# Optimization experiments

Hardware: AMD Instinct MI355X
Metric: run time of the kernel (lower is better)

Reference implementation:

```python
import jax, jax.numpy as jnp
import numpy as np

N_NODES = 50000
N_EDGES = 800000
F_IN = 64
HID = 128
N_GRAPHS = 64
F_OUT = 1
NEG_SLOPE = 0.2


def _glorot(key, shape):
    fan_in, fan_out = shape[0], shape[-1]
    s = jnp.sqrt(6.0 / (fan_in + fan_out))
    return jax.random.uniform(key, shape, jnp.float32, -s, s)


def setup_inputs() -> dict:
    key = jax.random.key(0)
    ks = jax.random.split(key, 24)
    inp = {
        "x": jax.random.normal(ks[0], (N_NODES, F_IN), jnp.float32),
        "edge_index": jax.random.randint(ks[1], (2, N_EDGES), 0, N_NODES, jnp.int32),
        "edge_weight": jax.random.uniform(ks[2], (N_EDGES, 1), jnp.float32),
        "batch": jnp.sort(jax.random.randint(ks[3], (N_NODES,), 0, N_GRAPHS, jnp.int32)),
        # GATv2Conv layer 1 (heads=1): lin_l, lin_r (with bias), lin_edge (no bias), att, out-bias
        "W1l": _glorot(ks[4], (F_IN, HID)), "b1l": jnp.zeros((HID,), jnp.float32),
        "W1r": _glorot(ks[5], (F_IN, HID)), "b1r": jnp.zeros((HID,), jnp.float32),
        "We1": _glorot(ks[6], (1, HID)),
        "att1": _glorot(ks[7], (HID, 1))[:, 0],
        "bias1": jnp.zeros((HID,), jnp.float32),
        # GATv2Conv layer 2
        "W2l": _glorot(ks[8], (HID, HID)), "b2l": jnp.zeros((HID,), jnp.float32),
        "W2r": _glorot(ks[9], (HID, HID)), "b2r": jnp.zeros((HID,), jnp.float32),
        "We2": _glorot(ks[10], (1, HID)),
        "att2": _glorot(ks[11], (HID, 1))[:, 0],
        "bias2": jnp.zeros((HID,), jnp.float32),
        # final Linear
        "Wlin": _glorot(ks[12], (HID, F_OUT)),
        "blin": jnp.zeros((F_OUT,), jnp.float32),
    }
    return inp


def gatv2_layer(x, src, dst, eattr, Wl, bl, Wr, br, We, att, bias):
    n = x.shape[0]
    # add_self_loops=True with edge_attr fill_value='mean'
    loop = jnp.arange(n, dtype=src.dtype)
    src = jnp.concatenate([src, loop])
    dst = jnp.concatenate([dst, loop])
    mean_attr = jnp.mean(eattr, axis=0, keepdims=True)  # [1, edge_dim]
    eattr = jnp.concatenate([eattr, jnp.broadcast_to(mean_attr, (n, eattr.shape[1]))])
    xl = x @ Wl + bl            # [N, HID] source transform
    xr = x @ Wr + br            # [N, HID] dest transform
    ee = eattr @ We             # [E', HID] edge embedding
    m = jax.nn.leaky_relu(xl[src] + xr[dst] + ee, NEG_SLOPE)  # [E', HID]
    logits = m @ att            # [E']
    # per-destination softmax (every node has a self loop, so no empty segments)
    lmax = jax.ops.segment_max(logits, dst, num_segments=n)
    w = jnp.exp(logits - lmax[dst])
    denom = jax.ops.segment_sum(w, dst, num_segments=n)
    alpha = w / denom[dst]
    out = jax.ops.segment_sum(xl[src] * alpha[:, None], dst, num_segments=n)
    return out + bias


def reference(x, edge_index, edge_weight, batch,
              W1l, b1l, W1r, b1r, We1, att1, bias1,
              W2l, b2l, W2r, b2r, We2, att2, bias2,
              Wlin, blin):
    src, dst = edge_index[0], edge_index[1]
    h = jax.nn.relu(gatv2_layer(x, src, dst, edge_weight, W1l, b1l, W1r, b1r, We1, att1, bias1))
    h = jax.nn.relu(gatv2_layer(h, src, dst, edge_weight, W2l, b2l, W2r, b2r, We2, att2, bias2))
    # global_mean_pool over graph assignment
    sums = jax.ops.segment_sum(h, batch, num_segments=N_GRAPHS)
    cnt = jax.ops.segment_sum(jnp.ones((h.shape[0],), h.dtype), batch, num_segments=N_GRAPHS)
    pooled = sums / jnp.maximum(cnt, 1.0)[:, None]
    return pooled @ Wlin + blin  # [N_GRAPHS, F_OUT]
```

## Files before the change

### kernel.cpp

```cpp
#include <hip/hip_runtime.h>

#define NN 50000
#define NE 800000
#define EP (NE + NN)
#define HID 128
#define FIN 64
#define NG 64
#define SLOPE 0.2f
#define NB 49

typedef unsigned short ushort_t;
typedef unsigned int uint_t;

__device__ __forceinline__ float wred_sum(float v) {
  for (int off = 32; off; off >>= 1) v += __shfl_xor(v, off);
  return v;
}
__device__ __forceinline__ ushort_t f2bf(float f) {
  uint_t b = __float_as_uint(f);
  b += 0x7fffu + ((b >> 16) & 1u);
  return (ushort_t)(b >> 16);
}

#define FMA4(A_, S_, W_) \
  A_.x += (S_) * W_.x; A_.y += (S_) * W_.y; \
  A_.z += (S_) * W_.z; A_.w += (S_) * W_.w;

__global__ void k_hist2(const int* __restrict__ edst, const float* __restrict__ ew,
                        int* __restrict__ counts, float* __restrict__ meansum) {
  int tid = blockIdx.x * blockDim.x + threadIdx.x;
  int stride = gridDim.x * blockDim.x;
  float s = 0.f;
  for (int i = tid; i < NE; i += stride) {
    atomicAdd(&counts[edst[i]], 1);
    s += ew[i];
  }
  s = wred_sum(s);
  if ((threadIdx.x & 63) == 0) atomicAdd(meansum, s);
}

__global__ __launch_bounds__(1024) void k_scan1(const int* __restrict__ counts,
                                                int* __restrict__ starts,
                                                int* __restrict__ bsum) {
  __shared__ int wsum[16];
  __shared__ int woff[16];
  int t = threadIdx.x, lane = t & 63, w = t >> 6;
  int i = blockIdx.x * 1024 + t;
  int v = (i < NN) ? counts[i] + 1 : 0;
  int sc = v;
  #pragma unroll
  for (int d = 1; d < 64; d <<= 1) {
    int u = __shfl_up(sc, d);
    if (lane >= d) sc += u;
  }
  if (lane == 63) wsum[w] = sc;
  __syncthreads();
  if (w == 0 && lane < 16) {
    int x = wsum[lane];
    #pragma unroll
    for (int d = 1; d < 16; d <<= 1) {
      int u = __shfl_up(x, d);
      if (lane >= d) x += u;
    }
    woff[lane] = x;
  }
  __syncthreads();
  int waveoff = (w == 0) ? 0 : woff[w - 1];
  if (i < NN) starts[i] = waveoff + sc - v;
  if (t == 1023) bsum[blockIdx.x] = woff[15];
}

__global__ void k_scan2(int* __restrict__ bsum, int* __restrict__ starts) {
  int t = threadIdx.x;
  int v = (t < NB) ? bsum[t] : 0;
  int sc = v;
  #pragma unroll
  for (int d = 1; d < 64; d <<= 1) {
    int u = __shfl_up(sc, d);
    if (t >= d) sc += u;
  }
  if (t < NB) bsum[t] = sc - v;
  if (t == 0) starts[NN] = EP;
}

__global__ __launch_bounds__(1024) void k_scan3(int* __restrict__ starts,
                                                const int* __restrict__ bsum,
                                                int* __restrict__ counts) {
  int i = blockIdx.x * 1024 + threadIdx.x;
  if (i < NN) {
    starts[i] += bsum[blockIdx.x];
    counts[i] = 0;
  }
}

__global__ void k_scatter(const int* __restrict__ esrc, const int* __restrict__ edst,
                          const float* __restrict__ ew, const float* __restrict__ meansum,
                          const int* __restrict__ starts, int* __restrict__ cursor,
                          int2* __restrict__ emeta) {
  float mw = meansum[0] * (1.0f / NE);
  int tid = blockIdx.x * blockDim.x + threadIdx.x;
  int stride = gridDim.x * blockDim.x;
  for (int i = tid; i < EP; i += stride) {
    int s, d; float wv;
    if (i < NE) { s = esrc[i]; d = edst[i]; wv = ew[i]; }
    else        { s = d = i - NE; wv = mw; }
    int pos = starts[d] + atomicAdd(&cursor[d], 1);
    emeta[pos] = make_int2(s, __float_as_int(wv));
  }
}

template <int K>
__global__ __launch_bounds__(256) void k_gemm2(const float* __restrict__ A,
                                               const float* __restrict__ Wl,
                                               const float* __restrict__ bl,
                                               const float* __restrict__ Wr,
                                               const float* __restrict__ br,
                                               ushort_t* __restrict__ xlout,
                                               float* __restrict__ xrout, int n) {
  __shared__ float As[64][K];
  int t = threadIdx.x;
  int nb = blockIdx.x * 64;
  constexpr int F4 = 16 * K;
  for (int i = t; i < F4; i += 256) {
    int row = i / (K / 4);
    int c = (i % (K / 4)) * 4;
    int gn = nb + row;
    float4 v = make_float4(0.f, 0.f, 0.f, 0.f);
    if (gn < n) v = *(const float4*)(A + (size_t)gn * K + c);
    *(float4*)&As[row][c] = v;
  }
  __syncthreads();
  int fx = (t & 31) * 4;
  int ny = (t >> 5) * 8;
  float4 accL[8], accR[8];
  #pragma unroll
  for (int j = 0; j < 8; ++j) {
    accL[j] = make_float4(0.f, 0.f, 0.f, 0.f);
    accR[j] = make_float4(0.f, 0.f, 0.f, 0.f);
  }
  for (int k4 = 0; k4 < K; k4 += 4) {
    float4 wl0 = *(const float4*)(Wl + (size_t)(k4 + 0) * HID + fx);
    float4 wl1 = *(const float4*)(Wl + (size_t)(k4 + 1) * HID + fx);
    float4 wl2 = *(const float4*)(Wl + (size_t)(k4 + 2) * HID + fx);
    float4 wl3 = *(const float4*)(Wl + (size_t)(k4 + 3) * HID + fx);
    float4 wr0 = *(const float4*)(Wr + (size_t)(k4 + 0) * HID + fx);
    float4 wr1 = *(const float4*)(Wr + (size_t)(k4 + 1) * HID + fx);
    float4 wr2 = *(const float4*)(Wr + (size_t)(k4 + 2) * HID + fx);
    float4 wr3 = *(const float4*)(Wr + (size_t)(k4 + 3) * HID + fx);
    #pragma unroll
    for (int j = 0; j < 8; ++j) {
      float4 a = *(const float4*)&As[ny + j][k4];
      FMA4(accL[j], a.x, wl0); FMA4(accL[j], a.y, wl1);
      FMA4(accL[j], a.z, wl2); FMA4(accL[j], a.w, wl3);
      FMA4(accR[j], a.x, wr0); FMA4(accR[j], a.y, wr1);
      FMA4(accR[j], a.z, wr2); FMA4(accR[j], a.w, wr3);
    }
  }
  float4 bbl = *(const float4*)(bl + fx);
  float4 bbr = *(const float4*)(br + fx);
  #pragma unroll
  for (int j = 0; j < 8; ++j) {
    int gn = nb + ny + j;
    if (gn < n) {
      ushort4 u4;
      u4.x = f2bf(accL[j].x + bbl.x); u4.y = f2bf(accL[j].y + bbl.y);
      u4.z = f2bf(accL[j].z + bbl.z); u4.w = f2bf(accL[j].w + bbl.w);
      *(ushort4*)(xlout + (size_t)gn * HID + fx) = u4;
      float4 o = make_float4(accR[j].x + bbr.x, accR[j].y + bbr.y,
                             accR[j].z + bbr.z, accR[j].w + bbr.w);
      *(float4*)(xrout + (size_t)gn * HID + fx) = o;
    }
  }
}

__global__ __launch_bounds__(256, 4) void k_fused(const ushort_t* __restrict__ xl16,
                                                  const float* __restrict__ xr,
                                                  const int2* __restrict__ emeta,
                                                  const int* __restrict__ starts,
                                                  const float* __restrict__ We,
                                                  const float* __restrict__ att,
                                                  const float* __restrict__ bias,
                                                  float* __restrict__ hout) {
  int node = blockIdx.x * (blockDim.x >> 6) + (threadIdx.x >> 6);
  int lane = threadIdx.x & 63;
  if (node >= NN) return;
  int hl = lane & 31;
  int half = lane >> 5;
  int s0 = starts[node], s1 = starts[node + 1];
  int f = hl * 4;
  float4 xro = *(const float4*)(xr + (size_t)node * HID + f);
  float4 we  = *(const float4*)(We + f);
  float4 at  = *(const float4*)(att + f);

  int emy = 8 * half + ((hl >> 2) & 7);
  bool b4 = (hl & 16) != 0;
  bool b3 = (hl & 8) != 0;
  bool b2 = (hl & 4) != 0;

  float ssum = 0.f;
  float4 acc = make_float4(0.f, 0.f, 0.f, 0.f);

  for (int i0 = s0; i0 < s1; i0 += 16) {
    int base = i0 + 8 * half;
    uint2 g[8];
    float p[8];
    #pragma unroll
    for (int k = 0; k < 8; ++k) {
      int idx = min(base + k, s1 - 1);
      int2 em = emeta[idx];
      p[k] = __int_as_float(em.y);
      g[k] = *(const uint2*)(xl16 + (size_t)em.x * HID + f);
    }
    #pragma unroll
    for (int k = 0; k < 8; ++k) {
      float wk = p[k];
      float t0 = __uint_as_float(g[k].x << 16)          + xro.x + wk * we.x;
      float t1 = __uint_as_float(g[k].x & 0xffff0000u)  + xro.y + wk * we.y;
      float t2 = __uint_as_float(g[k].y << 16)          + xro.z + wk * we.z;
      float t3 = __uint_as_float(g[k].y & 0xffff0000u)  + xro.w + wk * we.w;
      t0 = t0 > 0.f ? t0 : SLOPE * t0;
      t1 = t1 > 0.f ? t1 : SLOPE * t1;
      t2 = t2 > 0.f ? t2 : SLOPE * t2;
      t3 = t3 > 0.f ? t3 : SLOPE * t3;
      p[k] = t0 * at.x + t1 * at.y + t2 * at.z + t3 * at.w;
    }
    float sdv, rcv;
    float q0, q1, q2, q3;
    sdv = b4 ? p[0] : p[4]; rcv = __shfl_xor(sdv, 16, 32); q0 = (b4 ? p[4] : p[0]) + rcv;
    sdv = b4 ? p[1] : p[5]; rcv = __shfl_xor(sdv, 16, 32); q1 = (b4 ? p[5] : p[1]) + rcv;
    sdv = b4 ? p[2] : p[6]; rcv = __shfl_xor(sdv, 16, 32); q2 = (b4 ? p[6] : p[2]) + rcv;
    sdv = b4 ? p[3] : p[7]; rcv = __shfl_xor(sdv, 16, 32); q3 = (b4 ? p[7] : p[3]) + rcv;
    float r0, r1;
    sdv = b3 ? q0 : q2; rcv = __shfl_xor(sdv, 8, 32); r0 = (b3 ? q2 : q0) + rcv;
    sdv = b3 ? q1 : q3; rcv = __shfl_xor(sdv, 8, 32); r1 = (b3 ? q3 : q1) + rcv;
    sdv = b2 ? r0 : r1; rcv = __shfl_xor(sdv, 4, 32);
    float lg = (b2 ? r1 : r0) + rcv;
    lg += __shfl_xor(lg, 1, 32);
    lg += __shfl_xor(lg, 2, 32);
    float w = (i0 + emy < s1) ? __expf(lg) : 0.f;
    ssum += w;
    #pragma unroll
    for (int k = 0; k < 8; ++k) {
      float wk = __shfl(w, k << 2, 32);
      acc.x += wk * __uint_as_float(g[k].x << 16);
      acc.y += wk * __uint_as_float(g[k].x & 0xffff0000u);
      acc.z += wk * __uint_as_float(g[k].y << 16);
      acc.w += wk * __uint_as_float(g[k].y & 0xffff0000u);
    }
  }
  acc.x += __shfl_xor(acc.x, 32);
  acc.y += __shfl_xor(acc.y, 32);
  acc.z += __shfl_xor(acc.z, 32);
  acc.w += __shfl_xor(acc.w, 32);
  float st = wred_sum(ssum) * 0.25f;
  float inv = 1.0f / st;
  if (half == 0) {
    float4 bb = *(const float4*)(bias + f);
    float4 o;
    o.x = fmaxf(acc.x * inv + bb.x, 0.f);
    o.y = fmaxf(acc.y * inv + bb.y, 0.f);
    o.z = fmaxf(acc.z * inv + bb.z, 0.f);
    o.w = fmaxf(acc.w * inv + bb.w, 0.f);
    *(float4*)(hout + (size_t)node * HID + f) = o;
  }
}

__global__ void k_bounds(const int* __restrict__ batch, int* __restrict__ gs) {
  int i = blockIdx.x * blockDim.x + threadIdx.x;
  if (i >= NN) return;
  int b = batch[i];
  if (i == 0) {
    for (int g = 0; g <= b; ++g) gs[g] = 0;
  }
  int bn = (i + 1 < NN) ? batch[i + 1] : NG;
  for (int g = b + 1; g <= bn; ++g) gs[g] = i + 1;
}

__global__ __launch_bounds__(256) void k_pool(const float* __restrict__ h,
                                              const int* __restrict__ gs,
                                              const float* __restrict__ Wlin,
                                              const float* __restrict__ blin,
                                              float* __restrict__ out) {
  __shared__ float red[256];
  int g = blockIdx.x;
  int t = threadIdx.x;
  int f = t & 127;
  int half = t >> 7;
  int n0 = gs[g], n1 = gs[g + 1];
  float s0 = 0.f, s1 = 0.f, s2 = 0.f, s3 = 0.f;
  int n = n0 + half;
  for (; n + 6 < n1; n += 8) {
    s0 += h[(size_t)n * HID + f];
    s1 += h[(size_t)(n + 2) * HID + f];
    s2 += h[(size_t)(n + 4) * HID + f];
    s3 += h[(size_t)(n + 6) * HID + f];
  }
  for (; n < n1; n += 2) s0 += h[(size_t)n * HID + f];
  red[t] = (s0 + s1) + (s2 + s3);
  __syncthreads();
  if (t < 128) {
    float pooled = red[t] + red[t + 128];
    float cnt = (float)max(n1 - n0, 1);
    red[t] = (pooled / cnt) * Wlin[f];
  }
  __syncthreads();
  if (t < 64) {
    float v = red[t] + red[t + 64];
    v = wred_sum(v);
    if (t == 0) out[g] = v + blin[0];
  }
}

extern "C" void kernel_launch(void* const* d_in, const int* in_sizes, int n_in,
                              void* d_out, int out_size, void* d_ws, size_t ws_size,
                              hipStream_t stream) {
  const float* x     = (const float*)d_in[0];
  const int*   ei    = (const int*)d_in[1];
  const float* ew    = (const float*)d_in[2];
  const int*   batch = (const int*)d_in[3];
  const float* W1l = (const float*)d_in[4];
  const float* b1l = (const float*)d_in[5];
  const float* W1r = (const float*)d_in[6];
  const float* b1r = (const float*)d_in[7];
  const float* We1 = (const float*)d_in[8];
  const float* at1 = (const float*)d_in[9];
  const float* bi1 = (const float*)d_in[10];
  const float* W2l = (const float*)d_in[11];
  const float* b2l = (const float*)d_in[12];
  const float* W2r = (const float*)d_in[13];
  const float* b2r = (const float*)d_in[14];
  const float* We2 = (const float*)d_in[15];
  const float* at2 = (const float*)d_in[16];
  const float* bi2 = (const float*)d_in[17];
  const float* Wlin = (const float*)d_in[18];
  const float* blin = (const float*)d_in[19];

  float* ws = (float*)d_ws;
  size_t o = 0;
  float*    xr    = ws + o; o += (size_t)NN * HID;
  float*    hb    = ws + o; o += (size_t)NN * HID;
  ushort_t* xl16  = (ushort_t*)(ws + o); o += (size_t)NN * HID / 2;
  int2*     emeta = (int2*)(ws + o); o += (size_t)2 * EP;
  int*      starts = (int*)(ws + o); o += NN + 1;
  int*      gs     = (int*)(ws + o); o += NG + 1;
  int*      bsum   = (int*)(ws + o); o += NB;
  size_t zoff = o;
  int*      counts  = (int*)(ws + o); o += NN;
  float*    meansum = ws + o; o += 1;
  size_t zero_bytes = (o - zoff) * sizeof(float);

  hipMemsetAsync(counts, 0, zero_bytes, stream);

  k_hist2<<<1024, 256, 0, stream>>>(ei + NE, ew, counts, meansum);
  k_scan1<<<NB, 1024, 0, stream>>>(counts, starts, bsum);
  k_scan2<<<1, 64, 0, stream>>>(bsum, starts);
  k_scan3<<<NB, 1024, 0, stream>>>(starts, bsum, counts);
  k_scatter<<<1024, 256, 0, stream>>>(ei, ei + NE, ew, meansum, starts, counts,
                                      emeta);
  k_bounds<<<(NN + 255) / 256, 256, 0, stream>>>(batch, gs);

  int gb  = (NN + 63) / 64;
  int nbn = (NN + 3) / 4;

  k_gemm2<FIN><<<gb, 256, 0, stream>>>(x, W1l, b1l, W1r, b1r, xl16, xr, NN);
  k_fused<<<nbn, 256, 0, stream>>>(xl16, xr, emeta, starts, We1, at1, bi1, hb);
  k_gemm2<HID><<<gb, 256, 0, stream>>>(hb, W2l, b2l, W2r, b2r, xl16, xr, NN);
  k_fused<<<nbn, 256, 0, stream>>>(xl16, xr, emeta, starts, We2, at2, bi2, hb);
  k_pool<<<NG, 256, 0, stream>>>(hb, gs, Wlin, blin, (float*)d_out);
}
```

Before: 405.6 us.

## Use bf16 MFMA for node transforms and store hidden activations in bf16

Replaces the fp32 SIMT GEMM computing xl/xr with a bf16 MFMA 16x16x32 kernel. Inputs are converted to bf16 and the weights are packed into a K-blocked layout by small preprocessing kernels. Layer outputs h are now stored as bf16, which halves the traffic for the second GEMM and for pooling. The cost is lower precision and extra conversion and pack launches, and the epilogue now writes scalar, non-vectorized stores.

```diff
diff --git a/kernel.cpp b/kernel.cpp
--- a/kernel.cpp
+++ b/kernel.cpp
@@ -11,6 +11,8 @@
 
 typedef unsigned short ushort_t;
 typedef unsigned int uint_t;
+typedef __attribute__((ext_vector_type(8))) short bf16x8;
+typedef __attribute__((ext_vector_type(4))) float f32x4;
 
 __device__ __forceinline__ float wred_sum(float v) {
   for (int off = 32; off; off >>= 1) v += __shfl_xor(v, off);
@@ -21,10 +23,25 @@
   b += 0x7fffu + ((b >> 16) & 1u);
   return (ushort_t)(b >> 16);
 }
-
-#define FMA4(A_, S_, W_) \
-  A_.x += (S_) * W_.x; A_.y += (S_) * W_.y; \
-  A_.z += (S_) * W_.z; A_.w += (S_) * W_.w;
+__device__ __forceinline__ float bf2f(ushort_t u) {
+  return __uint_as_float((uint_t)u << 16);
+}
+
+__global__ void k_cvt(const float* __restrict__ x, ushort_t* __restrict__ x16) {
+  int i = blockIdx.x * blockDim.x + threadIdx.x;
+  float4 v = *(const float4*)(x + (size_t)i * 4);
+  ushort4 u;
+  u.x = f2bf(v.x); u.y = f2bf(v.y); u.z = f2bf(v.z); u.w = f2bf(v.w);
+  *(ushort4*)(x16 + (size_t)i * 4) = u;
+}
+
+__global__ void k_packW(const float* __restrict__ W, ushort_t* __restrict__ WP,
+                        int K) {
+  int i = blockIdx.x * blockDim.x + threadIdx.x;
+  if (i >= K * HID) return;
+  int k = i / HID, nn = i % HID;
+  WP[((size_t)(k >> 5) * HID + nn) * 32 + (k & 31)] = f2bf(W[i]);
+}
 
 __global__ void k_hist2(const int* __restrict__ edst, const float* __restrict__ ew,
                         int* __restrict__ counts, float* __restrict__ meansum) {
@@ -110,65 +127,46 @@
 }
 
 template <int K>
-__global__ __launch_bounds__(256) void k_gemm2(const float* __restrict__ A,
-                                               const float* __restrict__ Wl,
+__global__ __launch_bounds__(256) void k_gemmM(const ushort_t* __restrict__ A16,
+                                               const ushort_t* __restrict__ WPl,
                                                const float* __restrict__ bl,
-                                               const float* __restrict__ Wr,
+                                               const ushort_t* __restrict__ WPr,
                                                const float* __restrict__ br,
                                                ushort_t* __restrict__ xlout,
                                                float* __restrict__ xrout, int n) {
-  __shared__ float As[64][K];
   int t = threadIdx.x;
-  int nb = blockIdx.x * 64;
-  constexpr int F4 = 16 * K;
-  for (int i = t; i < F4; i += 256) {
-    int row = i / (K / 4);
-    int c = (i % (K / 4)) * 4;
-    int gn = nb + row;
-    float4 v = make_float4(0.f, 0.f, 0.f, 0.f);
-    if (gn < n) v = *(const float4*)(A + (size_t)gn * K + c);
-    *(float4*)&As[row][c] = v;
-  }
-  __syncthreads();
-  int fx = (t & 31) * 4;
-  int ny = (t >> 5) * 8;
-  float4 accL[8], accR[8];
-  #pragma unroll
-  for (int j = 0; j < 8; ++j) {
-    accL[j] = make_float4(0.f, 0.f, 0.f, 0.f);
-    accR[j] = make_float4(0.f, 0.f, 0.f, 0.f);
-  }
-  for (int k4 = 0; k4 < K; k4 += 4) {
-    float4 wl0 = *(const float4*)(Wl + (size_t)(k4 + 0) * HID + fx);
-    float4 wl1 = *(const float4*)(Wl + (size_t)(k4 + 1) * HID + fx);
-    float4 wl2 = *(const float4*)(Wl + (size_t)(k4 + 2) * HID + fx);
-    float4 wl3 = *(const float4*)(Wl + (size_t)(k4 + 3) * HID + fx);
-    float4 wr0 = *(const float4*)(Wr + (size_t)(k4 + 0) * HID + fx);
-    float4 wr1 = *(const float4*)(Wr + (size_t)(k4 + 1) * HID + fx);
-    float4 wr2 = *(const float4*)(Wr + (size_t)(k4 + 2) * HID + fx);
-    float4 wr3 = *(const float4*)(Wr + (size_t)(k4 + 3) * HID + fx);
-    #pragma unroll
-    for (int j = 0; j < 8; ++j) {
-      float4 a = *(const float4*)&As[ny + j][k4];
-      FMA4(accL[j], a.x, wl0); FMA4(accL[j], a.y, wl1);
-      FMA4(accL[j], a.z, wl2); FMA4(accL[j], a.w, wl3);
-      FMA4(accR[j], a.x, wr0); FMA4(accR[j], a.y, wr1);
-      FMA4(accR[j], a.z, wr2); FMA4(accR[j], a.w, wr3);
-    }
-  }
-  float4 bbl = *(const float4*)(bl + fx);
-  float4 bbr = *(const float4*)(br + fx);
-  #pragma unroll
-  for (int j = 0; j < 8; ++j) {
-    int gn = nb + ny + j;
-    if (gn < n) {
-      ushort4 u4;
-      u4.x = f2bf(accL[j].x + bbl.x); u4.y = f2bf(accL[j].y + bbl.y);
-      u4.z = f2bf(accL[j].z + bbl.z); u4.w = f2bf(accL[j].w + bbl.w);
-      *(ushort4*)(xlout + (size_t)gn * HID + fx) = u4;
-      float4 o = make_float4(accR[j].x + bbr.x, accR[j].y + bbr.y,
-                             accR[j].z + bbr.z, accR[j].w + bbr.w);
-      *(float4*)(xrout + (size_t)gn * HID + fx) = o;
+  int wave = t >> 6, lane = t & 63;
+  int m = lane & 15, kb = lane >> 4;
+  int row0 = blockIdx.x * 64 + wave * 16;
+  int ra = min(row0 + m, n - 1);
+  f32x4 acc[16];
+  #pragma unroll
+  for (int i = 0; i < 16; ++i) acc[i] = (f32x4)(0.f);
+  #pragma unroll
+  for (int kt = 0; kt < K / 32; ++kt) {
+    bf16x8 a = *(const bf16x8*)(A16 + (size_t)ra * K + kt * 32 + kb * 8);
+    #pragma unroll
+    for (int nf = 0; nf < 8; ++nf) {
+      bf16x8 bfr = *(const bf16x8*)(WPl + ((size_t)kt * HID + nf * 16 + m) * 32 + kb * 8);
+      acc[nf] = __builtin_amdgcn_mfma_f32_16x16x32_bf16(a, bfr, acc[nf], 0, 0, 0);
+    }
+    #pragma unroll
+    for (int nf = 0; nf < 8; ++nf) {
+      bf16x8 bfr = *(const bf16x8*)(WPr + ((size_t)kt * HID + nf * 16 + m) * 32 + kb * 8);
+      acc[8 + nf] = __builtin_amdgcn_mfma_f32_16x16x32_bf16(a, bfr, acc[8 + nf], 0, 0, 0);
+    }
+  }
+  #pragma unroll
+  for (int nf = 0; nf < 8; ++nf) {
+    int col = nf * 16 + m;
+    float bbl = bl[col], bbr = br[col];
+    #pragma unroll
+    for (int j = 0; j < 4; ++j) {
+      int r = row0 + kb * 4 + j;
+      if (r < n) {
+        xlout[(size_t)r * HID + col] = f2bf(acc[nf][j] + bbl);
+        xrout[(size_t)r * HID + col] = acc[8 + nf][j] + bbr;
+      }
     }
   }
 }
@@ -180,7 +178,7 @@
                                                   const float* __restrict__ We,
                                                   const float* __restrict__ att,
                                                   const float* __restrict__ bias,
-                                                  float* __restrict__ hout) {
+                                                  ushort_t* __restrict__ hout) {
   int node = blockIdx.x * (blockDim.x >> 6) + (threadIdx.x >> 6);
   int lane = threadIdx.x & 63;
   if (node >= NN) return;
@@ -256,12 +254,12 @@
   float inv = 1.0f / st;
   if (half == 0) {
     float4 bb = *(const float4*)(bias + f);
-    float4 o;
-    o.x = fmaxf(acc.x * inv + bb.x, 0.f);
-    o.y = fmaxf(acc.y * inv + bb.y, 0.f);
-    o.z = fmaxf(acc.z * inv + bb.z, 0.f);
-    o.w = fmaxf(acc.w * inv + bb.w, 0.f);
-    *(float4*)(hout + (size_t)node * HID + f) = o;
+    ushort4 u;
+    u.x = f2bf(fmaxf(acc.x * inv + bb.x, 0.f));
+    u.y = f2bf(fmaxf(acc.y * inv + bb.y, 0.f));
+    u.z = f2bf(fmaxf(acc.z * inv + bb.z, 0.f));
+    u.w = f2bf(fmaxf(acc.w * inv + bb.w, 0.f));
+    *(ushort4*)(hout + (size_t)node * HID + f) = u;
   }
 }
 
@@ -276,7 +274,7 @@
   for (int g = b + 1; g <= bn; ++g) gs[g] = i + 1;
 }
 
-__global__ __launch_bounds__(256) void k_pool(const float* __restrict__ h,
+__global__ __launch_bounds__(256) void k_pool(const ushort_t* __restrict__ h,
                                               const int* __restrict__ gs,
                                               const float* __restrict__ Wlin,
                                               const float* __restrict__ blin,
@@ -290,12 +288,12 @@
   float s0 = 0.f, s1 = 0.f, s2 = 0.f, s3 = 0.f;
   int n = n0 + half;
   for (; n + 6 < n1; n += 8) {
-    s0 += h[(size_t)n * HID + f];
-    s1 += h[(size_t)(n + 2) * HID + f];
-    s2 += h[(size_t)(n + 4) * HID + f];
-    s3 += h[(size_t)(n + 6) * HID + f];
-  }
-  for (; n < n1; n += 2) s0 += h[(size_t)n * HID + f];
+    s0 += bf2f(h[(size_t)n * HID + f]);
+    s1 += bf2f(h[(size_t)(n + 2) * HID + f]);
+    s2 += bf2f(h[(size_t)(n + 4) * HID + f]);
+    s3 += bf2f(h[(size_t)(n + 6) * HID + f]);
+  }
+  for (; n < n1; n += 2) s0 += bf2f(h[(size_t)n * HID + f]);
   red[t] = (s0 + s1) + (s2 + s3);
   __syncthreads();
   if (t < 128) {
@@ -338,8 +336,13 @@
   float* ws = (float*)d_ws;
   size_t o = 0;
   float*    xr    = ws + o; o += (size_t)NN * HID;
-  float*    hb    = ws + o; o += (size_t)NN * HID;
   ushort_t* xl16  = (ushort_t*)(ws + o); o += (size_t)NN * HID / 2;
+  ushort_t* hb16  = (ushort_t*)(ws + o); o += (size_t)NN * HID / 2;
+  ushort_t* x16   = (ushort_t*)(ws + o); o += (size_t)NN * FIN / 2;
+  ushort_t* WP1l  = (ushort_t*)(ws + o); o += (size_t)FIN * HID / 2;
+  ushort_t* WP1r  = (ushort_t*)(ws + o); o += (size_t)FIN * HID / 2;
+  ushort_t* WP2l  = (ushort_t*)(ws + o); o += (size_t)HID * HID / 2;
+  ushort_t* WP2r  = (ushort_t*)(ws + o); o += (size_t)HID * HID / 2;
   int2*     emeta = (int2*)(ws + o); o += (size_t)2 * EP;
   int*      starts = (int*)(ws + o); o += NN + 1;
   int*      gs     = (int*)(ws + o); o += NG + 1;
@@ -351,6 +354,12 @@
 
   hipMemsetAsync(counts, 0, zero_bytes, stream);
 
+  k_cvt<<<(NN * FIN / 4) / 256, 256, 0, stream>>>(x, x16);
+  k_packW<<<(FIN * HID + 255) / 256, 256, 0, stream>>>(W1l, WP1l, FIN);
+  k_packW<<<(FIN * HID + 255) / 256, 256, 0, stream>>>(W1r, WP1r, FIN);
+  k_packW<<<(HID * HID + 255) / 256, 256, 0, stream>>>(W2l, WP2l, HID);
+  k_packW<<<(HID * HID + 255) / 256, 256, 0, stream>>>(W2r, WP2r, HID);
+
   k_hist2<<<1024, 256, 0, stream>>>(ei + NE, ew, counts, meansum);
   k_scan1<<<NB, 1024, 0, stream>>>(counts, starts, bsum);
   k_scan2<<<1, 64, 0, stream>>>(bsum, starts);
@@ -362,9 +371,9 @@
   int gb  = (NN + 63) / 64;
   int nbn = (NN + 3) / 4;
 
-  k_gemm2<FIN><<<gb, 256, 0, stream>>>(x, W1l, b1l, W1r, b1r, xl16, xr, NN);
-  k_fused<<<nbn, 256, 0, stream>>>(xl16, xr, emeta, starts, We1, at1, bi1, hb);
-  k_gemm2<HID><<<gb, 256, 0, stream>>>(hb, W2l, b2l, W2r, b2r, xl16, xr, NN);
-  k_fused<<<nbn, 256, 0, stream>>>(xl16, xr, emeta, starts, We2, at2, bi2, hb);
-  k_pool<<<NG, 256, 0, stream>>>(hb, gs, Wlin, blin, (float*)d_out);
-}
+  k_gemmM<FIN><<<gb, 256, 0, stream>>>(x16, WP1l, b1l, WP1r, b1r, xl16, xr, NN);
+  k_fused<<<nbn, 256, 0, stream>>>(xl16, xr, emeta, starts, We1, at1, bi1, hb16);
+  k_gemmM<HID><<<gb, 256, 0, stream>>>(hb16, WP2l, b2l, WP2r, b2r, xl16, xr, NN);
+  k_fused<<<nbn, 256, 0, stream>>>(xl16, xr, emeta, starts, We2, at2, bi2, hb16);
+  k_pool<<<NG, 256, 0, stream>>>(hb16, gs, Wlin, blin, (float*)d_out);
+}
```

New measurement: 394.1 us. 2.8% less time.
